# Kernel optimization log

Hardware: AMD Instinct MI355X
Metric: run time of the kernel (lower is better)

Reference implementation:

```python
import jax, jax.numpy as jnp
import numpy as np

jax.config.update("jax_enable_x64", True)  # original uses complex128 FFTs

H0 = W0 = 3072   # full frame (shp_0)
HC = WC = 2048   # center_dims
MS_H = MS_W = 10
EPS = 1e-8


def setup_inputs() -> dict:
    key = jax.random.key(0)
    k1, k2 = jax.random.split(key)
    # smooth base image so the NCC peak neighborhood is positive (log-valid),
    # as the algorithm assumes for real microscopy data
    base = jax.image.resize(jax.random.normal(k1, (192, 192), jnp.float32), (H0, W0), method="linear")
    fr = jnp.roll(base, (3, -2), axis=(0, 1))[None, :, :, None] + 0.02 * jax.random.normal(k2, (1, H0, W0, 1), jnp.float32)
    template = base[:, :, None, None]
    return {"fr": fr.astype(jnp.float32), "template": template.astype(jnp.float32)}


def _avg_pool_valid(x, kh, kw):
    # x: (1,H,W,C); stride-1 VALID average pool via summed-area table (kernel is huge: ~2028x2028)
    s = jnp.cumsum(jnp.cumsum(x.astype(jnp.float64), axis=1), axis=2)
    s = jnp.pad(s, ((0, 0), (1, 0), (1, 0), (0, 0)))
    H, W = x.shape[1], x.shape[2]
    oh, ow = H - kh + 1, W - kw + 1
    sums = (s[:, kh:kh + oh, kw:kw + ow] - s[:, :oh, kw:kw + ow]
            - s[:, kh:kh + oh, :ow] + s[:, :oh, :ow])
    return (sums / (kh * kw)).astype(x.dtype)


def _extract_fractional_peak(ncc, ms_h, ms_w):
    n = ncc[0, :, :, 0]                     # (2*ms_w+1, 2*ms_h+1)
    W = n.shape[1]
    am = jnp.argmax(n.reshape(-1))
    sx = (am // W).astype(jnp.int32)
    sy = (am % W).astype(jnp.int32)
    log_n = jnp.log(n)
    lxm1 = log_n[sx - 1, sy]
    lxp1 = log_n[sx + 1, sy]
    lym1 = log_n[sx, sy - 1]
    lyp1 = log_n[sx, sy + 1]
    four = 4.0 * log_n[sx, sy]
    sh_x = -(sx - ms_h).astype(jnp.float32) - (lxm1 - lxp1) / (2.0 * lxm1 - four + 2.0 * lxp1)
    sh_y = -(sy - ms_w).astype(jnp.float32) - (lym1 - lyp1) / (2.0 * lym1 - four + 2.0 * lyp1)
    return sh_x.reshape(1, 1), sh_y.reshape(1, 1)


def _translate_bilinear(img, dx, dy):
    # tfa.image.translate semantics: out[r,c] = bilinear img[r - dy, c - dx], zero fill outside
    H, W = img.shape
    r = jnp.arange(H, dtype=img.dtype)[:, None] - dy   # (H,1)
    c = jnp.arange(W, dtype=img.dtype)[None, :] - dx   # (1,W)
    r0 = jnp.floor(r)
    c0 = jnp.floor(c)
    wr = r - r0
    wc = c - c0
    r0i = r0.astype(jnp.int32)
    c0i = c0.astype(jnp.int32)

    def samp(ri, ci):
        valid = (ri >= 0) & (ri < H) & (ci >= 0) & (ci < W)
        v = img[jnp.clip(ri, 0, H - 1), jnp.clip(ci, 0, W - 1)]  # index broadcast -> (H,W)
        return jnp.where(valid, v, jnp.zeros((), img.dtype))

    return (samp(r0i, c0i) * (1 - wr) * (1 - wc)
            + samp(r0i, c0i + 1) * (1 - wr) * wc
            + samp(r0i + 1, c0i) * wr * (1 - wc)
            + samp(r0i + 1, c0i + 1) * wr * wc)


def _forward(fr, template):
    scx = (H0 - HC) // 2
    scy = (W0 - WC) // 2
    tmpl = template[scx:H0 - scx, scy:W0 - scy]             # (HC,WC,1,1)
    shp_prod = float(HC * WC)
    mx, my = HC // 2, WC // 2

    # template normalization (done once in __init__ originally)
    t_zm = tmpl - jnp.mean(tmpl, axis=(0, 1), keepdims=True)
    t_var = jnp.sum(jnp.square(t_zm), axis=(0, 1), keepdims=True) + EPS   # (1,1,1,1)
    target_freq = jnp.fft.fftn(t_zm[:, :, :, 0].astype(jnp.complex128), axes=(0, 1, 2))

    fr_center = fr[0, scx:H0 - scx, scy:W0 - scy][None]     # (1,HC,WC,1)
    imgs_zm = fr_center - jnp.mean(fr_center, axis=(1, 2), keepdims=True)
    img_stack = jnp.stack([fr_center[:, :, :, 0], jnp.square(fr_center)[:, :, :, 0]], axis=3)
    local_mean = _avg_pool_valid(img_stack, HC - 2 * MS_W, WC - 2 * MS_H)  # (1,21,21,2)
    imgs_var = local_mean[..., 1:2] - jnp.square(local_mean[..., 0:1]) / shp_prod + EPS
    imgs_var = jnp.where(imgs_var < 0, jnp.zeros_like(imgs_var), imgs_var)
    denom = jnp.sqrt(t_var * imgs_var)                      # (1,21,21,1)

    fr_freq = jnp.fft.fftn(imgs_zm[0].astype(jnp.complex128), axes=(0, 1, 2))
    cc = jnp.abs(jnp.fft.ifftn(fr_freq * jnp.conj(target_freq), axes=(0, 1, 2))).astype(jnp.float32)[None]
    rolled = jnp.roll(cc, (mx, my), axis=(1, 2))
    ncc = rolled[:, mx - MS_W:mx + MS_W + 1, my - MS_H:my + MS_H + 1] / denom
    ncc = jnp.where(jnp.isnan(ncc), jnp.zeros_like(ncc), ncc)

    sh_x, sh_y = _extract_fractional_peak(ncc, MS_H, MS_W)
    fr_corr = _translate_bilinear(fr[0, :, :, 0], sh_x[0, 0], sh_y[0, 0])
    flat = jnp.reshape(fr_corr.T, (-1,))[None, :]
    return flat, sh_x, sh_y


def reference(fr, template):
    return _forward(fr, template)
```

## Files before the change

kernel.cpp:

```cpp
#include <hip/hip_runtime.h>
#include <math.h>

#define H0 3072
#define HC 2048
#define OFF 512
#define NA 21
#define NAB 441
#define KWIN 2028

#define TCH 64
#define YCB 128
#define NTB 32
#define NYB 16
#define NBLK (NTB * NYB)
#define ILDS_STR 136
#define ILDS_ROWS 95
#define ILDS_BYTES (ILDS_ROWS * ILDS_STR * 2)
#define T_ROWE 176
#define T_ROWW 88
#define CSTR_DW 2824
#define CSTR_E  5648
#define TLDS_BYTES (4 * CSTR_DW * 4)

#define WS_SCAL 128
#define WS_P1   4096
#define WS_RS   36864
#define WS_R    65536
#define WS_R2   409600
#define WS_DEN  753664
#define WS_CCV  757760
#define WS_CP   786432

typedef __attribute__((ext_vector_type(8))) short short8;
typedef __attribute__((ext_vector_type(4))) float f32x4;

static __device__ __forceinline__ unsigned f2bf_pack(float a, float b) {
    union { float f; unsigned u; } x, y; x.f = a; y.f = b;
    unsigned ra = (x.u + 0x7fff + ((x.u >> 16) & 1)) >> 16;
    unsigned rb = (y.u + 0x7fff + ((y.u >> 16) & 1)) >> 16;
    return ra | (rb << 16);
}

__global__ __launch_bounds__(256) void k_rowpool(const float* __restrict__ fr,
                          const float* __restrict__ tp,
                          double* __restrict__ Rv, double* __restrict__ Rv2,
                          double* __restrict__ rowsum, double* __restrict__ p1) {
    __shared__ float row[2048];
    __shared__ double s1[4], s2[4], s3[4], s4[4];
    int x = blockIdx.x, tid = threadIdx.x;
    const float* srcF = fr + (size_t)(OFF + x) * H0 + OFF;
    const float* srcT = tp + (size_t)(OFF + x) * H0 + OFF;
    float4 v0 = *(const float4*)&srcF[4 * tid];
    float4 v1 = *(const float4*)&srcF[4 * tid + 1024];
    *(float4*)&row[4 * tid] = v0;
    *(float4*)&row[4 * tid + 1024] = v1;
    double a = ((double)v0.x + v0.y) + ((double)v0.z + v0.w) +
               ((double)v1.x + v1.y) + ((double)v1.z + v1.w);
    double b = ((double)v0.x * v0.x + (double)v0.y * v0.y) +
               ((double)v0.z * v0.z + (double)v0.w * v0.w) +
               ((double)v1.x * v1.x + (double)v1.y * v1.y) +
               ((double)v1.z * v1.z + (double)v1.w * v1.w);
    float4 t0 = *(const float4*)&srcT[4 * tid];
    float4 t1 = *(const float4*)&srcT[4 * tid + 1024];
    double st = ((double)t0.x + t0.y) + ((double)t0.z + t0.w) +
                ((double)t1.x + t1.y) + ((double)t1.z + t1.w);
    double st2 = ((double)t0.x * t0.x + (double)t0.y * t0.y) +
                 ((double)t0.z * t0.z + (double)t0.w * t0.w) +
                 ((double)t1.x * t1.x + (double)t1.y * t1.y) +
                 ((double)t1.z * t1.z + (double)t1.w * t1.w);
    for (int o = 32; o > 0; o >>= 1) {
        a += __shfl_down(a, o); b += __shfl_down(b, o);
        st += __shfl_down(st, o); st2 += __shfl_down(st2, o);
    }
    if ((tid & 63) == 0) {
        int w = tid >> 6;
        s1[w] = a; s2[w] = b; s3[w] = st; s4[w] = st2;
    }
    __syncthreads();
    if (tid == 0) {
        double A = s1[0] + s1[1] + s1[2] + s1[3];
        double B = s2[0] + s2[1] + s2[2] + s2[3];
        rowsum[x] = A;
        p1[2 * x]     = s3[0] + s3[1] + s3[2] + s3[3];
        p1[2 * x + 1] = s4[0] + s4[1] + s4[2] + s4[3];
        s1[0] = A; s2[0] = B;
    }
    __syncthreads();
    if (tid < NA) {
        double h1 = 0, h2 = 0;
        for (int y = 0; y < tid; y++)          { float v = row[y]; h1 += v; h2 += (double)v * v; }
        for (int y = tid + KWIN; y < 2048; y++){ float v = row[y]; h1 += v; h2 += (double)v * v; }
        Rv [(size_t)tid * 2048 + x] = s1[0] - h1;
        Rv2[(size_t)tid * 2048 + x] = s2[0] - h2;
    }
}

__global__ void k_scal(const double* __restrict__ p1, const double* __restrict__ rowsum,
                       float* __restrict__ scal) {
    __shared__ double rs[512 * 3];
    int tid = threadIdx.x;
    double st = 0, st2 = 0, sf = 0;
    for (int k = 0; k < 4; k++) {
        int x = tid + 512 * k;
        st += p1[2 * x]; st2 += p1[2 * x + 1]; sf += rowsum[x];
    }
    rs[tid] = st; rs[512 + tid] = st2; rs[1024 + tid] = sf;
    __syncthreads();
    for (int off = 256; off > 0; off >>= 1) {
        if (tid < off) {
            rs[tid] += rs[tid + off];
            rs[512 + tid] += rs[512 + tid + off];
            rs[1024 + tid] += rs[1024 + tid + off];
        }
        __syncthreads();
    }
    if (tid == 0) {
        double N = (double)HC * (double)HC;
        double s = rs[0], s2 = rs[512], sfd = rs[1024];
        float mt = (float)(s / N);
        float mf = (float)(sfd / N);
        double m = (double)mt;
        double tv = s2 - 2.0 * m * s + N * m * m;
        scal[0] = mt;
        scal[1] = mf;
        scal[2] = (float)tv + 1e-8f;
    }
}

__global__ void k_dencol(const double* __restrict__ Rv, const double* __restrict__ Rv2,
                         const float* __restrict__ scal, float* __restrict__ den) {
    __shared__ double sm0[4], sm1[4];
    int j = blockIdx.x, tid = threadIdx.x;
    const double* R0 = Rv  + (size_t)j * 2048;
    const double* R1 = Rv2 + (size_t)j * 2048;
    double s0 = 0, s1 = 0;
    for (int x = tid; x < 2048; x += 256) { s0 += R0[x]; s1 += R1[x]; }
    for (int o = 32; o > 0; o >>= 1) { s0 += __shfl_down(s0, o); s1 += __shfl_down(s1, o); }
    if ((tid & 63) == 0) { sm0[tid >> 6] = s0; sm1[tid >> 6] = s1; }
    __syncthreads();
    if (tid < NA) {
        double T0 = sm0[0] + sm0[1] + sm0[2] + sm0[3];
        double T1 = sm1[0] + sm1[1] + sm1[2] + sm1[3];
        int i = tid;
        double h0 = 0, h1 = 0;
        for (int x = 0; x < i; x++)           { h0 += R0[x]; h1 += R1[x]; }
        for (int x = i + KWIN; x < 2048; x++) { h0 += R0[x]; h1 += R1[x]; }
        double area = (double)KWIN * (double)KWIN;
        float lm0 = (float)((T0 - h0) / area);
        float lm1 = (float)((T1 - h1) / area);
        float iv = lm1 - (lm0 * lm0) / 4194304.0f + 1e-8f;
        if (iv < 0.f) iv = 0.f;
        den[i * NA + j] = sqrtf(scal[2] * iv);
    }
}

__global__ __launch_bounds__(256) void k_corr(const float* __restrict__ fr,
                                              const float* __restrict__ tp,
                                              const float* __restrict__ scal,
                                              float* __restrict__ cp) {
    __shared__ __align__(16) char smem[ILDS_BYTES + TLDS_BYTES];
    unsigned short* Il = (unsigned short*)smem;
    unsigned short* Tl = (unsigned short*)(smem + ILDS_BYTES);
    unsigned* Iw = (unsigned*)smem;
    unsigned* Tw = (unsigned*)Tl;
    int tid = threadIdx.x;
    int bid = blockIdx.x;
    int t0 = (bid >> 4) * TCH;
    int y0 = (bid & 15) * YCB;
    float mt = scal[0], mf = scal[1];

    for (int idx = tid; idx < ILDS_ROWS * 32; idx += 256) {
        int row = idx >> 5, pc4 = idx & 31;
        int grow = (t0 - 10 + row) & (HC - 1);
        float4 v = *(const float4*)&fr[(size_t)(OFF + grow) * H0 + OFF + y0 + 4 * pc4];
        uint2 pk;
        pk.x = f2bf_pack(v.x - mf, v.y - mf);
        pk.y = f2bf_pack(v.z - mf, v.w - mf);
        *(uint2*)(Iw + row * (ILDS_STR / 2) + 2 * pc4) = pk;
    }

    int l = tid & 63, wv = tid >> 6;
    int kg = l >> 4, i16 = l & 15;
    f32x4 acc00 = {0.f, 0.f, 0.f, 0.f};
    f32x4 acc01 = {0.f, 0.f, 0.f, 0.f};
    f32x4 acc10 = {0.f, 0.f, 0.f, 0.f};
    f32x4 acc11 = {0.f, 0.f, 0.f, 0.f};

    for (int s = 0; s < 2; ++s) {
        for (int u = tid; u < 32 * 11; u += 256) {
            int row = u / 11, k = u - row * 11;
            int e0 = 16 * k;
            const float* srcT = tp + (size_t)(OFF + t0 + 32 * s + row) * H0 + OFF;
            unsigned w[10];
#pragma unroll
            for (int q4 = 0; q4 < 5; ++q4) {
                int gcol = (y0 - 24 + e0 + 4 * q4) & (HC - 1);
                float4 v = *(const float4*)&srcT[gcol];
                w[2 * q4]     = f2bf_pack(v.x - mt, v.y - mt);
                w[2 * q4 + 1] = f2bf_pack(v.z - mt, v.w - mt);
            }
            unsigned* dst = Tw + row * T_ROWW + 8 * k;
            uint4 c0a = {w[0], w[1], w[2], w[3]};
            uint4 c0b = {w[4], w[5], w[6], w[7]};
            *(uint4*)(dst) = c0a;
            *(uint4*)(dst + 4) = c0b;
            unsigned d1[8], d2[8], d3[8];
#pragma unroll
            for (int jj = 0; jj < 8; ++jj) {
                d1[jj] = (w[jj] >> 16) | (w[jj + 1] << 16);
                d2[jj] = w[jj + 1];
                d3[jj] = (w[jj + 1] >> 16) | (w[jj + 2] << 16);
            }
            uint4 c1a = {d1[0], d1[1], d1[2], d1[3]}, c1b = {d1[4], d1[5], d1[6], d1[7]};
            uint4 c2a = {d2[0], d2[1], d2[2], d2[3]}, c2b = {d2[4], d2[5], d2[6], d2[7]};
            uint4 c3a = {d3[0], d3[1], d3[2], d3[3]}, c3b = {d3[4], d3[5], d3[6], d3[7]};
            *(uint4*)(dst + CSTR_DW) = c1a;     *(uint4*)(dst + CSTR_DW + 4) = c1b;
            *(uint4*)(dst + 2 * CSTR_DW) = c2a; *(uint4*)(dst + 2 * CSTR_DW + 4) = c2b;
            *(uint4*)(dst + 3 * CSTR_DW) = c3a; *(uint4*)(dst + 3 * CSTR_DW + 4) = c3b;
        }
        __syncthreads();

        for (int dt = 0; dt < 8; ++dt) {
            int tl = 8 * wv + dt;
            const unsigned short* Trow = Tl + tl * T_ROWE;
            const unsigned short* Ir0 = Il + (32 * s + tl + i16) * ILDS_STR;
            const unsigned short* Ir1 = Ir0 + 16 * ILDS_STR;
#pragma unroll
            for (int ks = 0; ks < 4; ++ks) {
                int yk = 32 * ks + 8 * kg;
                short8 a0 = *(const short8*)(Ir0 + yk);
                short8 a1 = *(const short8*)(Ir1 + yk);
                union { uint2 u[2]; short8 s; } ub0, ub1;
                {
                    int s0 = yk - i16 + 34;
                    int c = s0 & 3;
                    const unsigned short* q = Trow + c * CSTR_E + (s0 - c);
                    ub0.u[0] = *(const uint2*)q;
                    ub0.u[1] = *(const uint2*)(q + 4);
                }
                {
                    int s0 = yk - i16 + 18;
                    int c = s0 & 3;
                    const unsigned short* q = Trow + c * CSTR_E + (s0 - c);
                    ub1.u[0] = *(const uint2*)q;
                    ub1.u[1] = *(const uint2*)(q + 4);
                }
                acc00 = __builtin_amdgcn_mfma_f32_16x16x32_bf16(a0, ub0.s, acc00, 0, 0, 0);
                acc01 = __builtin_amdgcn_mfma_f32_16x16x32_bf16(a0, ub1.s, acc01, 0, 0, 0);
                acc10 = __builtin_amdgcn_mfma_f32_16x16x32_bf16(a1, ub0.s, acc10, 0, 0, 0);
                acc11 = __builtin_amdgcn_mfma_f32_16x16x32_bf16(a1, ub1.s, acc11, 0, 0, 0);
            }
        }
        __syncthreads();
    }

    float* buf = (float*)smem;
    {
        int r0w = 4 * kg;
#pragma unroll
        for (int r = 0; r < 4; ++r) {
            buf[wv * 1024 + (r0w + r) * 32 + i16]           = acc00[r];
            buf[wv * 1024 + (r0w + r) * 32 + 16 + i16]      = acc01[r];
            buf[wv * 1024 + (16 + r0w + r) * 32 + i16]      = acc10[r];
            buf[wv * 1024 + (16 + r0w + r) * 32 + 16 + i16] = acc11[r];
        }
    }
    __syncthreads();
    for (int e = tid; e < 1024; e += 256) {
        int a = e >> 5, b = e & 31;
        if (a < NA && b < NA)
            cp[(size_t)bid * NAB + a * NA + b] =
                buf[e] + buf[1024 + e] + buf[2048 + e] + buf[3072 + e];
    }
}

__global__ void k_ccreduce(const float* __restrict__ cp, double* __restrict__ ccv) {
    __shared__ double red[256];
    int ab = blockIdx.x, tid = threadIdx.x;
    double s = 0;
    for (int blk = tid; blk < NBLK; blk += 256) s += (double)cp[(size_t)blk * NAB + ab];
    red[tid] = s;
    __syncthreads();
    for (int off = 128; off > 0; off >>= 1) {
        if (tid < off) red[tid] += red[tid + off];
        __syncthreads();
    }
    if (tid == 0) ccv[ab] = red[0];
}

__global__ void k_peak(const double* __restrict__ ccv, const float* __restrict__ den,
                       float* __restrict__ scal, float* __restrict__ out) {
    __shared__ float ncc[NAB];
    __shared__ float bv[512];
    __shared__ int bi_[512];
    int tid = threadIdx.x;
    if (tid < NAB) {
        float c = fabsf((float)ccv[tid]);
        float v = c / den[tid];
        if (v != v) v = 0.f;
        ncc[tid] = v;
    }
    __syncthreads();
    bv[tid] = (tid < NAB) ? ncc[tid] : -1e38f;
    bi_[tid] = (tid < NAB) ? tid : 0;
    __syncthreads();
    for (int off = 256; off > 0; off >>= 1) {
        if (tid < off) {
            float v2 = bv[tid + off]; int i2 = bi_[tid + off];
            if (v2 > bv[tid] || (v2 == bv[tid] && i2 < bi_[tid])) { bv[tid] = v2; bi_[tid] = i2; }
        }
        __syncthreads();
    }
    if (tid == 0) {
        int am = bi_[0];
        int sx = am / NA, sy = am - (am / NA) * NA;
        auto L = [&](int i, int j) {
            int ii = ((i % NA) + NA) % NA;
            int jj = ((j % NA) + NA) % NA;
            return logf(ncc[ii * NA + jj]);
        };
        float l0 = L(sx, sy);
        float lxm = L(sx - 1, sy), lxp = L(sx + 1, sy);
        float lym = L(sx, sy - 1), lyp = L(sx, sy + 1);
        float four = 4.f * l0;
        float shx = -(float)(sx - 10) - (lxm - lxp) / (2.f * lxm - four + 2.f * lxp);
        float shy = -(float)(sy - 10) - (lym - lyp) / (2.f * lym - four + 2.f * lyp);
        scal[3] = shx; scal[4] = shy;
        out[(size_t)H0 * H0]     = shx;
        out[(size_t)H0 * H0 + 1] = shy;
    }
}

__global__ __launch_bounds__(256) void k_translate(const float* __restrict__ fr,
                                                   const float* __restrict__ scal,
                                                   float* __restrict__ out) {
    __shared__ float T[65 * 67];
    int tid = threadIdx.x;
    int bx = blockIdx.x % 48, by = blockIdx.x / 48;
    int r0 = bx * 64, c0 = by * 64;
    float dx = scal[3], dy = scal[4];
    float fy = -dy, Fy = floorf(fy), wr = fy - Fy;
    float fx = -dx, Fx = floorf(fx), wc = fx - Fx;
    int R0 = r0 + (int)Fy, C0 = c0 + (int)Fx;
    for (int idx = tid; idx < 65 * 65; idx += 256) {
        int i = idx / 65, j = idx - i * 65;
        int gr = R0 + i, gc = C0 + j;
        float v = 0.f;
        if (gr >= 0 && gr < H0 && gc >= 0 && gc < H0) v = fr[(size_t)gr * H0 + gc];
        T[i * 67 + j] = v;
    }
    __syncthreads();
    float w00 = (1.f - wr) * (1.f - wc), w01 = (1.f - wr) * wc;
    float w10 = wr * (1.f - wc),        w11 = wr * wc;
    int rl = (tid & 15) * 4;
    int cl0 = tid >> 4;
    auto S = [&](int rr, int cl) {
        return w00 * T[rr * 67 + cl] + w01 * T[rr * 67 + cl + 1] +
               w10 * T[(rr + 1) * 67 + cl] + w11 * T[(rr + 1) * 67 + cl + 1];
    };
    for (int q = 0; q < 4; q++) {
        int cl = cl0 + q * 16;
        float4 res = make_float4(S(rl, cl), S(rl + 1, cl), S(rl + 2, cl), S(rl + 3, cl));
        *reinterpret_cast<float4*>(&out[(size_t)(c0 + cl) * H0 + r0 + rl]) = res;
    }
}

extern "C" void kernel_launch(void* const* d_in, const int* in_sizes, int n_in,
                              void* d_out, int out_size, void* d_ws, size_t ws_size,
                              hipStream_t stream) {
    const float* fr = (const float*)d_in[0];
    const float* tp = (const float*)d_in[1];
    float* out = (float*)d_out;
    char* ws = (char*)d_ws;
    float*  scal = (float*)(ws + WS_SCAL);
    double* p1   = (double*)(ws + WS_P1);
    double* rsum = (double*)(ws + WS_RS);
    double* Rv   = (double*)(ws + WS_R);
    double* Rv2  = (double*)(ws + WS_R2);
    float*  den  = (float*)(ws + WS_DEN);
    double* ccv  = (double*)(ws + WS_CCV);
    float*  cp   = (float*)(ws + WS_CP);

    k_rowpool   <<<2048, 256, 0, stream>>>(fr, tp, Rv, Rv2, rsum, p1);
    k_scal      <<<1, 512, 0, stream>>>(p1, rsum, scal);
    k_dencol    <<<NA, 256, 0, stream>>>(Rv, Rv2, scal, den);
    k_corr      <<<NBLK, 256, 0, stream>>>(fr, tp, scal, cp);
    k_ccreduce  <<<NAB, 256, 0, stream>>>(cp, ccv);
    k_peak      <<<1, 512, 0, stream>>>(ccv, den, scal, out);
    k_translate <<<2304, 256, 0, stream>>>(fr, scal, out);
}
```

Baseline: 71.16 us.

## Drop mean subtraction from correlation, correct algebraically, fold scalar kernel into dencol

Removes the single-block k_scal launch by computing the template and frame sums inside each k_dencol block, deriving the template variance there. k_corr no longer subtracts the means before bf16 packing. Because the correlation is cyclic, the mean terms are instead removed afterwards with a scalar constant C, which k_peak subtracts from every correlation value. This cuts one serialized launch and some arithmetic in the staging loops. The cost is bf16 rounding applied to raw rather than centered values, so accuracy relies on the means being small.

```diff
diff --git a/kernel.cpp b/kernel.cpp
--- a/kernel.cpp
+++ b/kernel.cpp
@@ -23,6 +23,7 @@
 #define TLDS_BYTES (4 * CSTR_DW * 4)
 
 #define WS_SCAL 128
+#define WS_CC0  192
 #define WS_P1   4096
 #define WS_RS   36864
 #define WS_R    65536
@@ -95,52 +96,38 @@
     }
 }
 
-__global__ void k_scal(const double* __restrict__ p1, const double* __restrict__ rowsum,
-                       float* __restrict__ scal) {
-    __shared__ double rs[512 * 3];
-    int tid = threadIdx.x;
-    double st = 0, st2 = 0, sf = 0;
-    for (int k = 0; k < 4; k++) {
-        int x = tid + 512 * k;
-        st += p1[2 * x]; st2 += p1[2 * x + 1]; sf += rowsum[x];
-    }
-    rs[tid] = st; rs[512 + tid] = st2; rs[1024 + tid] = sf;
-    __syncthreads();
-    for (int off = 256; off > 0; off >>= 1) {
-        if (tid < off) {
-            rs[tid] += rs[tid + off];
-            rs[512 + tid] += rs[512 + tid + off];
-            rs[1024 + tid] += rs[1024 + tid + off];
-        }
-        __syncthreads();
-    }
-    if (tid == 0) {
-        double N = (double)HC * (double)HC;
-        double s = rs[0], s2 = rs[512], sfd = rs[1024];
-        float mt = (float)(s / N);
-        float mf = (float)(sfd / N);
-        double m = (double)mt;
-        double tv = s2 - 2.0 * m * s + N * m * m;
-        scal[0] = mt;
-        scal[1] = mf;
-        scal[2] = (float)tv + 1e-8f;
-    }
-}
-
-__global__ void k_dencol(const double* __restrict__ Rv, const double* __restrict__ Rv2,
-                         const float* __restrict__ scal, float* __restrict__ den) {
-    __shared__ double sm0[4], sm1[4];
+__global__ __launch_bounds__(256) void k_dencol(const double* __restrict__ Rv,
+                         const double* __restrict__ Rv2,
+                         const double* __restrict__ p1, const double* __restrict__ rowsum,
+                         float* __restrict__ den, double* __restrict__ Cc) {
+    __shared__ double sm0[4], sm1[4], smt[4], smt2[4], smf[4];
     int j = blockIdx.x, tid = threadIdx.x;
     const double* R0 = Rv  + (size_t)j * 2048;
     const double* R1 = Rv2 + (size_t)j * 2048;
-    double s0 = 0, s1 = 0;
-    for (int x = tid; x < 2048; x += 256) { s0 += R0[x]; s1 += R1[x]; }
-    for (int o = 32; o > 0; o >>= 1) { s0 += __shfl_down(s0, o); s1 += __shfl_down(s1, o); }
-    if ((tid & 63) == 0) { sm0[tid >> 6] = s0; sm1[tid >> 6] = s1; }
+    double s0 = 0, s1 = 0, st = 0, st2 = 0, sf = 0;
+    for (int x = tid; x < 2048; x += 256) {
+        s0 += R0[x]; s1 += R1[x];
+        st += p1[2 * x]; st2 += p1[2 * x + 1]; sf += rowsum[x];
+    }
+    for (int o = 32; o > 0; o >>= 1) {
+        s0 += __shfl_down(s0, o); s1 += __shfl_down(s1, o);
+        st += __shfl_down(st, o); st2 += __shfl_down(st2, o); sf += __shfl_down(sf, o);
+    }
+    if ((tid & 63) == 0) {
+        int w = tid >> 6;
+        sm0[w] = s0; sm1[w] = s1; smt[w] = st; smt2[w] = st2; smf[w] = sf;
+    }
     __syncthreads();
     if (tid < NA) {
         double T0 = sm0[0] + sm0[1] + sm0[2] + sm0[3];
         double T1 = sm1[0] + sm1[1] + sm1[2] + sm1[3];
+        double ST = smt[0] + smt[1] + smt[2] + smt[3];
+        double ST2 = smt2[0] + smt2[1] + smt2[2] + smt2[3];
+        double SF = smf[0] + smf[1] + smf[2] + smf[3];
+        double N = (double)HC * (double)HC;
+        float mt = (float)(ST / N);
+        double m = (double)mt;
+        float tvar = (float)(ST2 - 2.0 * m * ST + N * m * m) + 1e-8f;
         int i = tid;
         double h0 = 0, h1 = 0;
         for (int x = 0; x < i; x++)           { h0 += R0[x]; h1 += R1[x]; }
@@ -150,13 +137,16 @@
         float lm1 = (float)((T1 - h1) / area);
         float iv = lm1 - (lm0 * lm0) / 4194304.0f + 1e-8f;
         if (iv < 0.f) iv = 0.f;
-        den[i * NA + j] = sqrtf(scal[2] * iv);
+        den[i * NA + j] = sqrtf(tvar * iv);
+        if (j == 0 && i == 0) {
+            float mf = (float)(SF / N);
+            *Cc = (double)mf * ST + (double)mt * SF - N * (double)mf * (double)mt;
+        }
     }
 }
 
 __global__ __launch_bounds__(256) void k_corr(const float* __restrict__ fr,
                                               const float* __restrict__ tp,
-                                              const float* __restrict__ scal,
                                               float* __restrict__ cp) {
     __shared__ __align__(16) char smem[ILDS_BYTES + TLDS_BYTES];
     unsigned short* Il = (unsigned short*)smem;
@@ -167,15 +157,14 @@
     int bid = blockIdx.x;
     int t0 = (bid >> 4) * TCH;
     int y0 = (bid & 15) * YCB;
-    float mt = scal[0], mf = scal[1];
 
     for (int idx = tid; idx < ILDS_ROWS * 32; idx += 256) {
         int row = idx >> 5, pc4 = idx & 31;
         int grow = (t0 - 10 + row) & (HC - 1);
         float4 v = *(const float4*)&fr[(size_t)(OFF + grow) * H0 + OFF + y0 + 4 * pc4];
         uint2 pk;
-        pk.x = f2bf_pack(v.x - mf, v.y - mf);
-        pk.y = f2bf_pack(v.z - mf, v.w - mf);
+        pk.x = f2bf_pack(v.x, v.y);
+        pk.y = f2bf_pack(v.z, v.w);
         *(uint2*)(Iw + row * (ILDS_STR / 2) + 2 * pc4) = pk;
     }
 
@@ -196,8 +185,8 @@
             for (int q4 = 0; q4 < 5; ++q4) {
                 int gcol = (y0 - 24 + e0 + 4 * q4) & (HC - 1);
                 float4 v = *(const float4*)&srcT[gcol];
-                w[2 * q4]     = f2bf_pack(v.x - mt, v.y - mt);
-                w[2 * q4 + 1] = f2bf_pack(v.z - mt, v.w - mt);
+                w[2 * q4]     = f2bf_pack(v.x, v.y);
+                w[2 * q4 + 1] = f2bf_pack(v.z, v.w);
             }
             unsigned* dst = Tw + row * T_ROWW + 8 * k;
             uint4 c0a = {w[0], w[1], w[2], w[3]};
@@ -289,13 +278,15 @@
 }
 
 __global__ void k_peak(const double* __restrict__ ccv, const float* __restrict__ den,
+                       const double* __restrict__ Cc,
                        float* __restrict__ scal, float* __restrict__ out) {
     __shared__ float ncc[NAB];
     __shared__ float bv[512];
     __shared__ int bi_[512];
     int tid = threadIdx.x;
+    double C = *Cc;
     if (tid < NAB) {
-        float c = fabsf((float)ccv[tid]);
+        float c = fabsf((float)(ccv[tid] - C));
         float v = c / den[tid];
         if (v != v) v = 0.f;
         ncc[tid] = v;
@@ -373,6 +364,7 @@
     float* out = (float*)d_out;
     char* ws = (char*)d_ws;
     float*  scal = (float*)(ws + WS_SCAL);
+    double* Cc   = (double*)(ws + WS_CC0);
     double* p1   = (double*)(ws + WS_P1);
     double* rsum = (double*)(ws + WS_RS);
     double* Rv   = (double*)(ws + WS_R);
@@ -382,10 +374,9 @@
     float*  cp   = (float*)(ws + WS_CP);
 
     k_rowpool   <<<2048, 256, 0, stream>>>(fr, tp, Rv, Rv2, rsum, p1);
-    k_scal      <<<1, 512, 0, stream>>>(p1, rsum, scal);
-    k_dencol    <<<NA, 256, 0, stream>>>(Rv, Rv2, scal, den);
-    k_corr      <<<NBLK, 256, 0, stream>>>(fr, tp, scal, cp);
+    k_dencol    <<<NA, 256, 0, stream>>>(Rv, Rv2, p1, rsum, den, Cc);
+    k_corr      <<<NBLK, 256, 0, stream>>>(fr, tp, cp);
     k_ccreduce  <<<NAB, 256, 0, stream>>>(cp, ccv);
-    k_peak      <<<1, 512, 0, stream>>>(ccv, den, scal, out);
+    k_peak      <<<1, 512, 0, stream>>>(ccv, den, Cc, scal, out);
     k_translate <<<2304, 256, 0, stream>>>(fr, scal, out);
 }
```

Result: faster. 68.66 us (-3.5%).
